# Kernel optimization log

Measured on AMD Instinct MI355X. Metric: run time of the kernel, lower is better.

## Reference

```python
import jax, jax.numpy as jnp
import numpy as np

D_MODEL = 1024
NUM_HEADS = 16
HEAD_DIM = D_MODEL // NUM_HEADS


def setup_inputs() -> dict:
    key = jax.random.key(0)
    k_x, k_wqkv, k_bqkv, k_wo, k_bo = jax.random.split(key, 5)
    B, T = 4, 2048
    s = 1.0 / np.sqrt(D_MODEL)
    return {
        "x": jax.random.normal(k_x, (B, T, D_MODEL), dtype=jnp.float32),
        "w_qkv": jax.random.uniform(k_wqkv, (D_MODEL, 3 * D_MODEL), jnp.float32, -s, s),
        "b_qkv": jax.random.uniform(k_bqkv, (3 * D_MODEL,), jnp.float32, -s, s),
        "w_out": jax.random.uniform(k_wo, (D_MODEL, D_MODEL), jnp.float32, -s, s),
        "b_out": jax.random.uniform(k_bo, (D_MODEL,), jnp.float32, -s, s),
    }


def reference(x, w_qkv, b_qkv, w_out, b_out):
    B, T, _ = x.shape
    H, Dh = NUM_HEADS, HEAD_DIM
    scale = Dh ** -0.5
    qkv = x @ w_qkv + b_qkv                       # [B,T,3D]
    qkv = qkv.reshape(B, T, 3, H, Dh)
    q = jnp.transpose(qkv[:, :, 0], (0, 2, 1, 3))  # [B,H,T,Dh]
    k = jnp.transpose(qkv[:, :, 1], (0, 2, 1, 3))
    v = jnp.transpose(qkv[:, :, 2], (0, 2, 1, 3))
    scores = jnp.einsum('bhqd,bhkd->bhqk', q, k) * scale
    causal = jnp.tril(jnp.ones((T, T), dtype=bool))
    scores = jnp.where(causal, scores, -jnp.inf)
    w = jax.nn.softmax(scores, axis=-1)
    out = jnp.einsum('bhqk,bhkd->bhqd', w, v)     # [B,H,T,Dh]
    out = jnp.transpose(out, (0, 2, 1, 3)).reshape(B, T, H * Dh)
    return out @ w_out + b_out
```

## Files before the change

kernel.cpp:

```cpp
#include <hip/hip_runtime.h>

typedef unsigned short u16;
typedef unsigned u32;
typedef float f32x4 __attribute__((ext_vector_type(4)));
typedef __bf16 bf16x8 __attribute__((ext_vector_type(8)));
typedef __bf16 bf16x2 __attribute__((ext_vector_type(2)));
typedef u32 u32x4 __attribute__((ext_vector_type(4)));
typedef u16 u16x4 __attribute__((ext_vector_type(4)));
typedef int i32x2 __attribute__((ext_vector_type(2)));

#define MFMA_16x16x32(a, b, c) __builtin_amdgcn_mfma_f32_16x16x32_bf16((a), (b), (c), 0, 0, 0)

#if __has_builtin(__builtin_amdgcn_exp2f)
#define EXP2(x) __builtin_amdgcn_exp2f(x)
#else
#define EXP2(x) exp2f(x)
#endif


__device__ __forceinline__ u16 f2bf(float f) {
  unsigned u = __builtin_bit_cast(unsigned, f);
  unsigned r = ((u >> 16) & 1u) + 0x7FFFu;
  return (u16)((u + r) >> 16);
}

__device__ __forceinline__ u32 pk2(float x, float y) {
  bf16x2 v = {(__bf16)x, (__bf16)y};
  return __builtin_bit_cast(u32, v);
}

__device__ __forceinline__ void gload16(const void* g, void* l) {
  __builtin_amdgcn_global_load_lds(
      (const __attribute__((address_space(1))) void*)g,
      (__attribute__((address_space(3))) void*)l, 16, 0, 0);
}


__global__ void cvt_to_bf16(const float* __restrict__ in, u16* __restrict__ out, int n) {
  const int i = (blockIdx.x * 256 + threadIdx.x) * 8;
  if (i >= n) return;
  const f32x4 a = *(const f32x4*)(in + i);
  const f32x4 b = *(const f32x4*)(in + i + 4);
  u16x4 u0, u1;
#pragma unroll
  for (int j = 0; j < 4; ++j) { u0[j] = f2bf(a[j]); u1[j] = f2bf(b[j]); }
  *(u16x4*)(out + i) = u0;
  *(u16x4*)(out + i + 4) = u1;
}

__global__ void transpose_cvt(const float* __restrict__ in, u16* __restrict__ out,
                              int rows, int cols) {
  __shared__ float t[64][65];
  const int rb = blockIdx.y * 64, cb = blockIdx.x * 64;
  for (int i = threadIdx.x; i < 4096; i += 256) {
    const int r = i >> 6, c = i & 63;
    t[r][c] = in[(size_t)(rb + r) * cols + cb + c];
  }
  __syncthreads();
  for (int i = threadIdx.x; i < 4096; i += 256) {
    const int r = i >> 6, c = i & 63;
    out[(size_t)(cb + r) * rows + rb + c] = f2bf(t[c][r]);
  }
}

template <int EPI>
__global__ __launch_bounds__(256, 2) void gemm_bt(
    const u16* __restrict__ A, const u16* __restrict__ Bt, int K,
    const float* __restrict__ bias,
    u16* __restrict__ oq, u16* __restrict__ ok, u16* __restrict__ ov,
    float* __restrict__ of, int N, int nbx) {
  __shared__ __align__(16) u16 As[128 * 32];
  __shared__ __align__(16) u16 Bs[128 * 32];
  const int tid = threadIdx.x;
  const int lane = tid & 63, w = tid >> 6;
  const int g = lane >> 4, cc = lane & 15;
  const int wr = w >> 1, wc = w & 1;
  const int bid = blockIdx.x;
  const int bx = bid % nbx, by = bid / nbx;

  const u16* pa = A + (size_t)(by * 128 + (tid >> 2)) * K + (tid & 3) * 8;
  const u16* pb = Bt + (size_t)(bx * 128 + (tid >> 2)) * K + (tid & 3) * 8;
  u16* la = &As[tid * 8];
  u16* lb = &Bs[tid * 8];
  const size_t rowskip = (size_t)64 * K;

  f32x4 acc[4][4] = {};
  const int aoff = (wr * 64 + cc) * 32 + g * 8;
  const int boff = (wc * 64 + cc) * 32 + g * 8;

  for (int k0 = 0; k0 < K; k0 += 32) {
    gload16(pa + k0, la);
    gload16(pa + rowskip + k0, la + 2048);
    gload16(pb + k0, lb);
    gload16(pb + rowskip + k0, lb + 2048);
    __syncthreads();
    bf16x8 af[4], bf[4];
#pragma unroll
    for (int mi = 0; mi < 4; ++mi) af[mi] = *(const bf16x8*)&As[aoff + mi * 512];
#pragma unroll
    for (int ni = 0; ni < 4; ++ni) bf[ni] = *(const bf16x8*)&Bs[boff + ni * 512];
#pragma unroll
    for (int mi = 0; mi < 4; ++mi)
#pragma unroll
      for (int ni = 0; ni < 4; ++ni)
        acc[mi][ni] = MFMA_16x16x32(af[mi], bf[ni], acc[mi][ni]);
    __syncthreads();
  }

  const int m00 = by * 128 + wr * 64 + 4 * g;
  const int n00 = bx * 128 + wc * 64;
#pragma unroll
  for (int ni = 0; ni < 4; ++ni) {
    const int n = n00 + ni * 16 + cc;
    const float bn = bias[n];
    if constexpr (EPI == 0) {
      const int which = n >> 10;
      const int d = n & 1023;
      const int h = d >> 6, dh = d & 63;
#pragma unroll
      for (int mi = 0; mi < 4; ++mi) {
        const int mb = m00 + mi * 16;
        const int b = mb >> 11, t = mb & 2047;
        if (which == 2) {
          u16x4 pk;
#pragma unroll
          for (int r = 0; r < 4; ++r) pk[r] = f2bf(acc[mi][ni][r] + bn);
          const int tt = (t & ~12) | ((t & 4) << 1) | ((t & 8) >> 1);
          *(u16x4*)&ov[((size_t)((b * 16 + h) * 64 + dh)) * 2048 + tt] = pk;
        } else {
          u16* dst = (which == 0 ? oq : ok) + ((size_t)((b * 16 + h) * 2048 + t)) * 64 + dh;
#pragma unroll
          for (int r = 0; r < 4; ++r) dst[(size_t)r * 64] = f2bf(acc[mi][ni][r] + bn);
        }
      }
    } else {
#pragma unroll
      for (int mi = 0; mi < 4; ++mi) {
        const int m = m00 + mi * 16;
#pragma unroll
        for (int r = 0; r < 4; ++r) of[(size_t)(m + r) * N + n] = acc[mi][ni][r] + bn;
      }
    }
  }
}

__global__ __launch_bounds__(256, 4) void flash_attn(
    const u16* __restrict__ Qb, const u16* __restrict__ Kb,
    const u16* __restrict__ Vt, u16* __restrict__ Ob) {
  __shared__ __align__(16) u16 Ks[8192];
  __shared__ __align__(16) u16 Vs[8192];

  const int bid = blockIdx.x;
  const int tq4 = bid >> 6, t0 = tq4 & 3, ti = tq4 >> 2;
  const int qt = (ti == 0) ? 15 - t0 : (ti == 1) ? 8 + t0 : (ti == 2) ? 7 - t0 : t0;
  const int bh = bid & 63;
  const int tid = threadIdx.x;
  const int lane = tid & 63, w = tid >> 6;
  const int g = lane >> 4, cc = lane & 15;
  const int q0 = qt * 128 + w * 32;

  bf16x8 bq[2][2];
  {
    const u16* qp = Qb + ((size_t)bh * 2048 + q0 + cc) * 64 + g * 8;
#pragma unroll
    for (int mi = 0; mi < 2; ++mi)
#pragma unroll
      for (int dc = 0; dc < 2; ++dc)
        bq[mi][dc] = *(const bf16x8*)(qp + (size_t)mi * 16 * 64 + dc * 32);
  }

  const char* kp[4];
  const char* vp[4];
  u16* kl[4];
  u16* vl[4];
  {
    const char* kbase = (const char*)(Kb + (size_t)bh * 2048 * 64);
    const char* vbase = (const char*)(Vt + (size_t)bh * 64 * 2048);
#pragma unroll
    for (int i = 0; i < 4; ++i) {
      const int f = i * 4 + w, ki = f & 7, dc = f >> 3;
      kp[i] = kbase + ((ki * 16 + cc) * 64 + dc * 32 + g * 8) * 2;
      vp[i] = vbase + ((w * 16 + cc) * 2048 + (4 * i + g) * 8) * 2;
      kl[i] = &Ks[f * 512 + lane * 8];
      vl[i] = &Vs[f * 512 + lane * 8];
    }
  }
  const u16* krd = &Ks[lane * 8];
  const u16* vrd = &Vs[lane * 8];

  f32x4 acc[2][4] = {};
  float m_run[2] = {-1e30f, -1e30f};
  float l_run[2] = {0.f, 0.f};
  const float sc = 0.18033688011112042f;

  for (int kt = 0; kt <= qt; ++kt) {
    __syncthreads();
#pragma unroll
    for (int i = 0; i < 4; ++i) gload16(kp[i], kl[i]);
#pragma unroll
    for (int i = 0; i < 4; ++i) gload16(vp[i], vl[i]);
#pragma unroll
    for (int i = 0; i < 4; ++i) { kp[i] += 128 * 64 * 2; vp[i] += 128 * 2; }
    __syncthreads();

#pragma unroll
    for (int mi = 0; mi < 2; ++mi) {
      f32x4 s[8] = {};
      __builtin_amdgcn_s_setprio(1);
#pragma unroll
      for (int dc = 0; dc < 2; ++dc) {
        const bf16x8 qf = bq[mi][dc];
#pragma unroll
        for (int ki = 0; ki < 8; ++ki) {
          const bf16x8 ak = *(const bf16x8*)(krd + (dc * 8 + ki) * 512);
          s[ki] = MFMA_16x16x32(ak, qf, s[ki]);
        }
      }
      __builtin_amdgcn_s_setprio(0);

      if (kt == qt) {
        const int qq = w * 32 + mi * 16 + cc;
#pragma unroll
        for (int ki = 0; ki < 8; ++ki) {
          const int kb_ = ki * 16 + 4 * g;
#pragma unroll
          for (int r = 0; r < 4; ++r)
            if (kb_ + r > qq) s[ki][r] = -1e30f;
        }
      }

      float mx = fmaxf(fmaxf(s[0][0], s[0][1]), fmaxf(s[0][2], s[0][3]));
#pragma unroll
      for (int ki = 1; ki < 8; ++ki)
        mx = fmaxf(mx, fmaxf(fmaxf(s[ki][0], s[ki][1]), fmaxf(s[ki][2], s[ki][3])));
      mx = fmaxf(mx, __shfl_xor(mx, 16));
      mx = fmaxf(mx, __shfl_xor(mx, 32));
      const float pm = mx * sc;

      if (!__all(pm - m_run[mi] <= 8.f)) {
        const float mn = fmaxf(m_run[mi], pm);
        const float sf = EXP2(m_run[mi] - mn);
        m_run[mi] = mn;
        l_run[mi] *= sf;
        float sfr[4];
#pragma unroll
        for (int r = 0; r < 4; ++r) sfr[r] = __shfl(sf, (lane & 48) + 4 * g + r);
#pragma unroll
        for (int ni = 0; ni < 4; ++ni)
#pragma unroll
          for (int r = 0; r < 4; ++r) acc[mi][ni][r] *= sfr[r];
      }
      const float mcur = m_run[mi];

      f32x4 rsv = {};
#pragma unroll
      for (int ko = 0; ko < 4; ++ko) {
        f32x4 pe, po;
#pragma unroll
        for (int r = 0; r < 4; ++r) {
          pe[r] = EXP2(__builtin_fmaf(s[2 * ko][r], sc, -mcur));
          po[r] = EXP2(__builtin_fmaf(s[2 * ko + 1][r], sc, -mcur));
        }
        rsv += pe;
        rsv += po;
        const u32 aw = pk2(pe[0], pe[1]), bw2 = pk2(pe[2], pe[3]);
        const u32 cw = pk2(po[0], po[1]), dw = pk2(po[2], po[3]);
#if __has_builtin(__builtin_amdgcn_permlane32_swap)
        const i32x2 s1 = __builtin_amdgcn_permlane32_swap((int)aw, (int)cw, false, false);
        const i32x2 s2 = __builtin_amdgcn_permlane32_swap((int)bw2, (int)dw, false, false);
        const u32x4 wv = {(u32)s1[0], (u32)s2[0], (u32)s1[1], (u32)s2[1]};
#else
        const bool lo2 = (g < 2);
        const u32 r_ac = __shfl_xor(lo2 ? cw : aw, 32);
        const u32 r_bd = __shfl_xor(lo2 ? dw : bw2, 32);
        const u32x4 wv = {lo2 ? aw : r_ac, lo2 ? bw2 : r_bd,
                          lo2 ? r_ac : cw, lo2 ? r_bd : dw};
#endif
        const bf16x8 pf = __builtin_bit_cast(bf16x8, wv);
        __builtin_amdgcn_s_setprio(1);
#pragma unroll
        for (int ni = 0; ni < 4; ++ni) {
          const bf16x8 bv = *(const bf16x8*)(vrd + (ko * 4 + ni) * 512);
          acc[mi][ni] = MFMA_16x16x32(pf, bv, acc[mi][ni]);
        }
        __builtin_amdgcn_s_setprio(0);
      }
      float rs = (rsv[0] + rsv[1]) + (rsv[2] + rsv[3]);
      rs += __shfl_xor(rs, 16);
      rs += __shfl_xor(rs, 32);
      l_run[mi] += rs;
    }
  }

  const int b = bh >> 4, h = bh & 15;
#pragma unroll
  for (int mi = 0; mi < 2; ++mi) {
    float inv[4];
#pragma unroll
    for (int r = 0; r < 4; ++r)
      inv[r] = 1.f / __shfl(l_run[mi], (lane & 48) + 4 * g + r);
#pragma unroll
    for (int ni = 0; ni < 4; ++ni)
#pragma unroll
      for (int r = 0; r < 4; ++r) {
        const int tq = q0 + mi * 16 + 4 * g + r;
        Ob[((size_t)(b * 2048 + tq)) * 1024 + h * 64 + ni * 16 + cc] =
            f2bf(acc[mi][ni][r] * inv[r]);
      }
  }
}


extern "C" void kernel_launch(void* const* d_in, const int* in_sizes, int n_in,
                              void* d_out, int out_size, void* d_ws, size_t ws_size,
                              hipStream_t stream) {
  const float* x     = (const float*)d_in[0];
  const float* w_qkv = (const float*)d_in[1];
  const float* b_qkv = (const float*)d_in[2];
  const float* w_out = (const float*)d_in[3];
  const float* b_out = (const float*)d_in[4];
  float* out = (float*)d_out;
  char* ws = (char*)d_ws;

  u16* xb    = (u16*)(ws + 0);
  u16* wqkvT = (u16*)(ws + 16777216);
  u16* woutT = (u16*)(ws + 23068672);
  u16* qbuf  = (u16*)(ws + 25165824);
  u16* kbuf  = (u16*)(ws + 41943040);
  u16* vbuf  = (u16*)(ws + 58720256);

  cvt_to_bf16<<<4096, 256, 0, stream>>>(x, xb, 8388608);
  transpose_cvt<<<dim3(48, 16), 256, 0, stream>>>(w_qkv, wqkvT, 1024, 3072);
  transpose_cvt<<<dim3(16, 16), 256, 0, stream>>>(w_out, woutT, 1024, 1024);
  gemm_bt<0><<<24 * 64, 256, 0, stream>>>(xb, wqkvT, 1024, b_qkv,
                                          qbuf, kbuf, vbuf, nullptr, 3072, 24);
  flash_attn<<<1024, 256, 0, stream>>>(qbuf, kbuf, vbuf, xb);
  gemm_bt<1><<<8 * 64, 256, 0, stream>>>(xb, woutT, 1024, b_out,
                                         nullptr, nullptr, nullptr, out, 1024, 8);
}
```

Before: 191.0 us.

## Double-buffer GEMM LDS tiles, remap block order, and reorder LDS layout

The bf16 GEMM used for the QKV and output projections now double-buffers its A and B shared-memory tiles. The next k-slice's global-to-LDS load is issued before the MFMAs on the current slice, and there is one barrier per iteration instead of two. The block index is remapped across 8 groups, likely to spread neighbouring tiles across XCDs for L2 locality, and the LDS layout changes so each wave reads its fragments contiguously by lane. MFMA sections are wrapped in s_setprio, at the cost of doubling shared memory per block, which may reduce occupancy.

```diff
diff --git a/kernel.cpp b/kernel.cpp
--- a/kernel.cpp
+++ b/kernel.cpp
@@ -69,42 +69,78 @@
     const float* __restrict__ bias,
     u16* __restrict__ oq, u16* __restrict__ ok, u16* __restrict__ ov,
     float* __restrict__ of, int N, int nbx) {
-  __shared__ __align__(16) u16 As[128 * 32];
-  __shared__ __align__(16) u16 Bs[128 * 32];
+  __shared__ __align__(16) u16 As[2][4096];
+  __shared__ __align__(16) u16 Bs[2][4096];
   const int tid = threadIdx.x;
   const int lane = tid & 63, w = tid >> 6;
   const int g = lane >> 4, cc = lane & 15;
   const int wr = w >> 1, wc = w & 1;
-  const int bid = blockIdx.x;
+
+  const int cpx = gridDim.x >> 3;
+  const int bid = ((int)blockIdx.x & 7) * cpx + ((int)blockIdx.x >> 3);
   const int bx = bid % nbx, by = bid / nbx;
 
-  const u16* pa = A + (size_t)(by * 128 + (tid >> 2)) * K + (tid & 3) * 8;
-  const u16* pb = Bt + (size_t)(bx * 128 + (tid >> 2)) * K + (tid & 3) * 8;
-  u16* la = &As[tid * 8];
-  u16* lb = &Bs[tid * 8];
-  const size_t rowskip = (size_t)64 * K;
+  const u16* pa = A + (size_t)(by * 128 + w * 16 + cc) * K + g * 8;
+  const u16* pb = Bt + (size_t)(bx * 128 + w * 16 + cc) * K + g * 8;
+  const size_t half = (size_t)64 * K;
+
+  u16* lda0 = &As[0][tid * 8];
+  u16* lda1 = &As[0][(tid + 256) * 8];
+  u16* ldb0 = &Bs[0][tid * 8];
+  u16* ldb1 = &Bs[0][(tid + 256) * 8];
+
+  const u16* ard = &As[0][(wr * 4) * 512 + lane * 8];
+  const u16* brd = &Bs[0][(wc * 4) * 512 + lane * 8];
 
   f32x4 acc[4][4] = {};
-  const int aoff = (wr * 64 + cc) * 32 + g * 8;
-  const int boff = (wc * 64 + cc) * 32 + g * 8;
-
-  for (int k0 = 0; k0 < K; k0 += 32) {
-    gload16(pa + k0, la);
-    gload16(pa + rowskip + k0, la + 2048);
-    gload16(pb + k0, lb);
-    gload16(pb + rowskip + k0, lb + 2048);
-    __syncthreads();
+
+  gload16(pa, lda0);
+  gload16(pa + half, lda1);
+  gload16(pb, ldb0);
+  gload16(pb + half, ldb1);
+  __syncthreads();
+
+  int cur = 0;
+  for (int k0 = 32; k0 < K; k0 += 32) {
+    const int nb = cur ^ 1;
+    const int off = nb * 4096;
+    gload16(pa + k0, lda0 + off);
+    gload16(pa + half + k0, lda1 + off);
+    gload16(pb + k0, ldb0 + off);
+    gload16(pb + half + k0, ldb1 + off);
+
+    const u16* ab = ard + cur * 4096;
+    const u16* bb = brd + cur * 4096;
     bf16x8 af[4], bf[4];
 #pragma unroll
-    for (int mi = 0; mi < 4; ++mi) af[mi] = *(const bf16x8*)&As[aoff + mi * 512];
-#pragma unroll
-    for (int ni = 0; ni < 4; ++ni) bf[ni] = *(const bf16x8*)&Bs[boff + ni * 512];
+    for (int mi = 0; mi < 4; ++mi) af[mi] = *(const bf16x8*)(ab + mi * 512);
+#pragma unroll
+    for (int ni = 0; ni < 4; ++ni) bf[ni] = *(const bf16x8*)(bb + ni * 512);
+    __builtin_amdgcn_s_setprio(1);
 #pragma unroll
     for (int mi = 0; mi < 4; ++mi)
 #pragma unroll
       for (int ni = 0; ni < 4; ++ni)
         acc[mi][ni] = MFMA_16x16x32(af[mi], bf[ni], acc[mi][ni]);
+    __builtin_amdgcn_s_setprio(0);
     __syncthreads();
+    cur = nb;
+  }
+  {
+    const u16* ab = ard + cur * 4096;
+    const u16* bb = brd + cur * 4096;
+    bf16x8 af[4], bf[4];
+#pragma unroll
+    for (int mi = 0; mi < 4; ++mi) af[mi] = *(const bf16x8*)(ab + mi * 512);
+#pragma unroll
+    for (int ni = 0; ni < 4; ++ni) bf[ni] = *(const bf16x8*)(bb + ni * 512);
+    __builtin_amdgcn_s_setprio(1);
+#pragma unroll
+    for (int mi = 0; mi < 4; ++mi)
+#pragma unroll
+      for (int ni = 0; ni < 4; ++ni)
+        acc[mi][ni] = MFMA_16x16x32(af[mi], bf[ni], acc[mi][ni]);
+    __builtin_amdgcn_s_setprio(0);
   }
 
   const int m00 = by * 128 + wr * 64 + 4 * g;
```

Result: slower. 240.0 us (+25.7%).

## Pipeline GEMM K-loop with 4-stage LDS ring buffer and XCD-aware block swizzle

Applied to the files above, without the earlier changes.

The GEMM main loop moves from one LDS buffer with two barriers per K-step to a 4-stage ring buffer. Global-to-LDS loads are issued three stages ahead and gated by explicit vmcnt waits, so memory latency overlaps the MFMA work. It also changes the LDS tile layout to match the MFMA fragment order, raises wave priority around the MFMAs, and remaps block IDs so neighbouring tiles land on the same XCD. The fully unrolled schedule hardcodes K=1024, and LDS use rises to 64KB per block, which can lower occupancy.

```diff
diff --git a/kernel.cpp b/kernel.cpp
--- a/kernel.cpp
+++ b/kernel.cpp
@@ -69,43 +69,75 @@
     const float* __restrict__ bias,
     u16* __restrict__ oq, u16* __restrict__ ok, u16* __restrict__ ov,
     float* __restrict__ of, int N, int nbx) {
-  __shared__ __align__(16) u16 As[128 * 32];
-  __shared__ __align__(16) u16 Bs[128 * 32];
+  __shared__ __align__(16) u16 As[4][4096];
+  __shared__ __align__(16) u16 Bs[4][4096];
   const int tid = threadIdx.x;
   const int lane = tid & 63, w = tid >> 6;
   const int g = lane >> 4, cc = lane & 15;
   const int wr = w >> 1, wc = w & 1;
-  const int bid = blockIdx.x;
+
+  const int cpx = gridDim.x >> 3;
+  const int bid = ((int)blockIdx.x & 7) * cpx + ((int)blockIdx.x >> 3);
   const int bx = bid % nbx, by = bid / nbx;
 
-  const u16* pa = A + (size_t)(by * 128 + (tid >> 2)) * K + (tid & 3) * 8;
-  const u16* pb = Bt + (size_t)(bx * 128 + (tid >> 2)) * K + (tid & 3) * 8;
-  u16* la = &As[tid * 8];
-  u16* lb = &Bs[tid * 8];
-  const size_t rowskip = (size_t)64 * K;
+  const u16* pa = A + (size_t)(by * 128 + w * 16 + cc) * K + g * 8;
+  const u16* pb = Bt + (size_t)(bx * 128 + w * 16 + cc) * K + g * 8;
+  const size_t half = (size_t)64 * K;
+
+  u16* la0 = &As[0][tid * 8];
+  u16* la1 = &As[0][(tid + 256) * 8];
+  u16* lb0 = &Bs[0][tid * 8];
+  u16* lb1 = &Bs[0][(tid + 256) * 8];
+  const u16* ard = &As[0][(wr * 4) * 512 + lane * 8];
+  const u16* brd = &Bs[0][(wc * 4) * 512 + lane * 8];
 
   f32x4 acc[4][4] = {};
-  const int aoff = (wr * 64 + cc) * 32 + g * 8;
-  const int boff = (wc * 64 + cc) * 32 + g * 8;
-
-  for (int k0 = 0; k0 < K; k0 += 32) {
-    gload16(pa + k0, la);
-    gload16(pa + rowskip + k0, la + 2048);
-    gload16(pb + k0, lb);
-    gload16(pb + rowskip + k0, lb + 2048);
-    __syncthreads();
-    bf16x8 af[4], bf[4];
-#pragma unroll
-    for (int mi = 0; mi < 4; ++mi) af[mi] = *(const bf16x8*)&As[aoff + mi * 512];
-#pragma unroll
-    for (int ni = 0; ni < 4; ++ni) bf[ni] = *(const bf16x8*)&Bs[boff + ni * 512];
-#pragma unroll
-    for (int mi = 0; mi < 4; ++mi)
-#pragma unroll
-      for (int ni = 0; ni < 4; ++ni)
-        acc[mi][ni] = MFMA_16x16x32(af[mi], bf[ni], acc[mi][ni]);
-    __syncthreads();
-  }
+
+#define STAGE(s, k0)                             \
+  do {                                           \
+    gload16(pa + (k0), la0 + (s) * 4096);        \
+    gload16(pa + half + (k0), la1 + (s) * 4096); \
+    gload16(pb + (k0), lb0 + (s) * 4096);        \
+    gload16(pb + half + (k0), lb1 + (s) * 4096); \
+  } while (0)
+
+#define COMPUTE(s)                                                \
+  do {                                                            \
+    bf16x8 af[4], bf[4];                                          \
+    _Pragma("unroll") for (int mi = 0; mi < 4; ++mi)              \
+        af[mi] = *(const bf16x8*)(ard + (s) * 4096 + mi * 512);   \
+    _Pragma("unroll") for (int ni = 0; ni < 4; ++ni)              \
+        bf[ni] = *(const bf16x8*)(brd + (s) * 4096 + ni * 512);   \
+    __builtin_amdgcn_s_setprio(1);                                \
+    _Pragma("unroll") for (int mi = 0; mi < 4; ++mi)              \
+      _Pragma("unroll") for (int ni = 0; ni < 4; ++ni)            \
+          acc[mi][ni] = MFMA_16x16x32(af[mi], bf[ni], acc[mi][ni]); \
+    __builtin_amdgcn_s_setprio(0);                                \
+  } while (0)
+
+#define WAITVM(n) asm volatile("s_waitcnt vmcnt(" #n ")" ::: "memory")
+#define BAR() __builtin_amdgcn_s_barrier()
+
+  STAGE(0, 0);
+  STAGE(1, 32);
+  STAGE(2, 64);
+
+  for (int j = 0; j < 7; ++j) {
+    const int kb = j * 128 + 96;
+    WAITVM(8); BAR(); STAGE(3, kb);      COMPUTE(0);
+    WAITVM(8); BAR(); STAGE(0, kb + 32); COMPUTE(1);
+    WAITVM(8); BAR(); STAGE(1, kb + 64); COMPUTE(2);
+    WAITVM(8); BAR(); STAGE(2, kb + 96); COMPUTE(3);
+  }
+  WAITVM(8); BAR(); STAGE(3, 992); COMPUTE(0);
+  WAITVM(8); BAR(); COMPUTE(1);
+  WAITVM(4); BAR(); COMPUTE(2);
+  WAITVM(0); BAR(); COMPUTE(3);
+
+#undef STAGE
+#undef COMPUTE
+#undef WAITVM
+#undef BAR
 
   const int m00 = by * 128 + wr * 64 + 4 * g;
   const int n00 = bx * 128 + wc * 64;
```

Result: slower. 234.8 us (+23.0%).

## Reorder GEMM LDS layout for conflict-free reads, swizzle blocks, raise occupancy

Applied to the files above, without the earlier changes.

The GEMM's LDS tile layout changes so each thread's global-to-LDS chunk lands in MFMA fragment order. Each lane then reads its fragment at a contiguous lane*8 offset, which should reduce LDS bank conflicts. Block IDs are remapped across 8 groups (likely XCD-aware) to improve L2 locality, and launch bounds go up to 4 blocks per SM. s_setprio is raised around the MFMA cluster. The higher occupancy target may constrain registers and cause spills with the 64-float accumulator.

```diff
diff --git a/kernel.cpp b/kernel.cpp
--- a/kernel.cpp
+++ b/kernel.cpp
@@ -64,46 +64,53 @@
 }
 
 template <int EPI>
-__global__ __launch_bounds__(256, 2) void gemm_bt(
+__global__ __launch_bounds__(256, 4) void gemm_bt(
     const u16* __restrict__ A, const u16* __restrict__ Bt, int K,
     const float* __restrict__ bias,
     u16* __restrict__ oq, u16* __restrict__ ok, u16* __restrict__ ov,
     float* __restrict__ of, int N, int nbx) {
-  __shared__ __align__(16) u16 As[128 * 32];
-  __shared__ __align__(16) u16 Bs[128 * 32];
+  __shared__ __align__(16) u16 As[4096];
+  __shared__ __align__(16) u16 Bs[4096];
   const int tid = threadIdx.x;
   const int lane = tid & 63, w = tid >> 6;
   const int g = lane >> 4, cc = lane & 15;
   const int wr = w >> 1, wc = w & 1;
-  const int bid = blockIdx.x;
+
+  const int cpx = gridDim.x >> 3;
+  const int bid = ((int)blockIdx.x & 7) * cpx + ((int)blockIdx.x >> 3);
   const int bx = bid % nbx, by = bid / nbx;
 
-  const u16* pa = A + (size_t)(by * 128 + (tid >> 2)) * K + (tid & 3) * 8;
-  const u16* pb = Bt + (size_t)(bx * 128 + (tid >> 2)) * K + (tid & 3) * 8;
-  u16* la = &As[tid * 8];
-  u16* lb = &Bs[tid * 8];
-  const size_t rowskip = (size_t)64 * K;
+  const u16* pa = A + (size_t)(by * 128 + w * 16 + cc) * K + g * 8;
+  const u16* pb = Bt + (size_t)(bx * 128 + w * 16 + cc) * K + g * 8;
+  const size_t half = (size_t)64 * K;
+
+  u16* la0 = &As[tid * 8];
+  u16* la1 = &As[(tid + 256) * 8];
+  u16* lb0 = &Bs[tid * 8];
+  u16* lb1 = &Bs[(tid + 256) * 8];
+  const u16* ard = &As[(wr * 4) * 512 + lane * 8];
+  const u16* brd = &Bs[(wc * 4) * 512 + lane * 8];
 
   f32x4 acc[4][4] = {};
-  const int aoff = (wr * 64 + cc) * 32 + g * 8;
-  const int boff = (wc * 64 + cc) * 32 + g * 8;
 
   for (int k0 = 0; k0 < K; k0 += 32) {
-    gload16(pa + k0, la);
-    gload16(pa + rowskip + k0, la + 2048);
-    gload16(pb + k0, lb);
-    gload16(pb + rowskip + k0, lb + 2048);
+    gload16(pa + k0, la0);
+    gload16(pa + half + k0, la1);
+    gload16(pb + k0, lb0);
+    gload16(pb + half + k0, lb1);
     __syncthreads();
     bf16x8 af[4], bf[4];
 #pragma unroll
-    for (int mi = 0; mi < 4; ++mi) af[mi] = *(const bf16x8*)&As[aoff + mi * 512];
-#pragma unroll
-    for (int ni = 0; ni < 4; ++ni) bf[ni] = *(const bf16x8*)&Bs[boff + ni * 512];
+    for (int mi = 0; mi < 4; ++mi) af[mi] = *(const bf16x8*)(ard + mi * 512);
+#pragma unroll
+    for (int ni = 0; ni < 4; ++ni) bf[ni] = *(const bf16x8*)(brd + ni * 512);
+    __builtin_amdgcn_s_setprio(1);
 #pragma unroll
     for (int mi = 0; mi < 4; ++mi)
 #pragma unroll
       for (int ni = 0; ni < 4; ++ni)
         acc[mi][ni] = MFMA_16x16x32(af[mi], bf[ni], acc[mi][ni]);
+    __builtin_amdgcn_s_setprio(0);
     __syncthreads();
   }
 
```

New measurement: 240.2 us. 1.26x slower.
